# Performance work log

Hardware: AMD Instinct MI355X
Metric: run time of the kernel (lower is better)

## Reference

```python
import jax, jax.numpy as jnp
import numpy as np

N_NODES = 50000
N_EDGES = 800000
F_IN, D1, N_CLS = 128, 128, 64


def gcn_conv(x, W, b, src, dst, n):
    # x: [N, Fin] -> linear transform then normalized scatter-add aggregation
    h = x @ W  # [N, Fout]
    deg = jnp.zeros((n,), h.dtype).at[dst].add(jnp.ones((dst.shape[0],), h.dtype))
    dis = jnp.where(deg > 0, jax.lax.rsqrt(jnp.maximum(deg, 1.0)), 0.0)  # deg^-1/2, inf->0
    norm = dis[src] * dis[dst]  # [E_tot]
    msgs = norm[:, None] * h[src]  # gather source features, scale by sym norm
    out = jax.ops.segment_sum(msgs, dst, num_segments=n)  # scatter-add to targets
    return out + b


def setup_inputs() -> dict:
    key = jax.random.key(0)
    ks = jax.random.split(key, 6)
    x = jax.random.normal(ks[0], (N_NODES, F_IN), dtype=jnp.float32)
    edge_index = jax.random.randint(ks[1], (2, N_EDGES), 0, N_NODES, dtype=jnp.int64)
    W1 = jax.random.normal(ks[2], (F_IN, D1), dtype=jnp.float32) / np.sqrt(F_IN)
    b1 = jnp.zeros((D1,), dtype=jnp.float32)
    W2 = jax.random.normal(ks[3], (D1, N_CLS), dtype=jnp.float32) / np.sqrt(D1)
    b2 = jnp.zeros((N_CLS,), dtype=jnp.float32)
    return {"x": x, "edge_index": edge_index, "W1": W1, "b1": b1, "W2": W2, "b2": b2}


def reference(x, edge_index, W1, b1, W2, b2):
    n = x.shape[0]
    loops = jnp.arange(n, dtype=edge_index.dtype)
    src = jnp.concatenate([edge_index[0], loops])  # add self-loops (PyG default)
    dst = jnp.concatenate([edge_index[1], loops])
    h = gcn_conv(x, W1, b1, src, dst, n)
    h = jax.nn.relu(h)
    # F.dropout(training=self.training) is identity in eval mode
    out = gcn_conv(h, W2, b2, src, dst, n)
    return out
```

## Files before the change

### kernel.cpp

```cpp
#include <hip/hip_runtime.h>

#define NN 50000
#define NE 800000
#define CAP 64
#define NPAD 50176
#define SLICE 6250

typedef unsigned int   u32;
typedef unsigned short u16;
typedef __attribute__((ext_vector_type(8))) short short8;
typedef __attribute__((ext_vector_type(4))) float f32x4;

__device__ inline u16 f2bf(float f) {
    u32 u = __float_as_uint(f);
    return (u16)((u + 0x7FFF + ((u >> 16) & 1)) >> 16);
}
__device__ inline float bfval(u16 h) { return __uint_as_float(((u32)h) << 16); }
__device__ inline float bf_lo(u32 u) { return __uint_as_float(u << 16); }
__device__ inline float bf_hi(u32 u) { return __uint_as_float(u & 0xFFFF0000u); }


__global__ __launch_bounds__(256) void build_ell(const int* __restrict__ ei,
                                                 int* __restrict__ cnt,
                                                 u16* __restrict__ ell) {
    const int s  = blockIdx.x & 7;
    const int g  = blockIdx.x >> 3;
    const int ng = gridDim.x >> 3;
    const int lo = s * SLICE, hi = lo + SLICE;
    for (int e0 = (g * 256 + (int)threadIdx.x) * 4; e0 < NE; e0 += ng * 1024) {
        int4 d4 = *(const int4*)(ei + NE + e0);
        int dv[4] = {d4.x, d4.y, d4.z, d4.w};
#pragma unroll
        for (int k = 0; k < 4; ++k) {
            int d = dv[k];
            if (d >= lo && d < hi) {
                int src = ei[e0 + k];
                int sh = k & 1;
                int pos = atomicAdd(&cnt[sh * NPAD + d], 1);
                if (pos < 32) ell[d * CAP + sh * 32 + pos] = (u16)src;
            }
        }
    }
}


__global__ __launch_bounds__(256) void prep_w(const float* __restrict__ W1,
                                              const float* __restrict__ W2,
                                              u16* __restrict__ W1h, u16* __restrict__ W1l,
                                              u16* __restrict__ W2h, u16* __restrict__ W2l,
                                              int* __restrict__ cnt) {
    int i = blockIdx.x * 256 + threadIdx.x;
    for (int z = i; z < 2 * NPAD; z += 32768) cnt[z] = 0;
    const float* W; u16 *Dh, *Dl; int NOUT, idx;
    if (i < 16384) { W = W1; Dh = W1h; Dl = W1l; NOUT = 128; idx = i; }
    else           { idx = i - 16384; if (idx >= 8192) return;
                     W = W2; Dh = W2h; Dl = W2l; NOUT = 64; }
    int j = idx & 7, l = (idx >> 3) & 63, kc = (idx >> 9) & 3, t = idx >> 11;
    int k = kc * 32 + (l >> 4) * 8 + j;
    int n = t * 16 + (l & 15);
    float w = W[k * NOUT + n];
    u16 h = f2bf(w);
    Dh[idx] = h;
    Dl[idx] = f2bf(w - bfval(h));
}


__global__ __launch_bounds__(256) void gemm_mfma1(const float* __restrict__ A,
                                                  const u16* __restrict__ Wh,
                                                  const u16* __restrict__ Wl,
                                                  u16* __restrict__ C, int M,
                                                  const int* __restrict__ cnt,
                                                  u16* __restrict__ degT) {
    constexpr int NT = 8;
    const int tid = threadIdx.x;

    if (tid < 64) {
        int node = blockIdx.x * 64 + tid;
        if (node < NN) degT[node] = (u16)(cnt[node] + cnt[NPAD + node] + 1);
    }

    const int w = tid >> 6, l = tid & 63;
    const int m = l & 15, q = l >> 4;

    int arow = blockIdx.x * 64 + w * 16 + m;
    const float* Ar = A + (size_t)min(arow, M - 1) * 128;

    f32x4 acc[NT] = {};

#pragma unroll
    for (int kc = 0; kc < 4; ++kc) {
        float p[8];
        *(float4*)&p[0] = *(const float4*)(Ar + kc * 32 + q * 8);
        *(float4*)&p[4] = *(const float4*)(Ar + kc * 32 + q * 8 + 4);
        short8 ah, al;
#pragma unroll
        for (int j = 0; j < 8; ++j) {
            u16 h = f2bf(p[j]);
            ah[j] = (short)h;
            al[j] = (short)f2bf(p[j] - bfval(h));
        }
#pragma unroll
        for (int t = 0; t < NT; ++t) {
            size_t bo = ((size_t)(t * 4 + kc) * 64 + l) * 8;
            short8 bh = *(const short8*)(Wh + bo);
            short8 bl = *(const short8*)(Wl + bo);
            acc[t] = __builtin_amdgcn_mfma_f32_16x16x32_bf16(ah, bh, acc[t], 0, 0, 0);
            acc[t] = __builtin_amdgcn_mfma_f32_16x16x32_bf16(al, bh, acc[t], 0, 0, 0);
            acc[t] = __builtin_amdgcn_mfma_f32_16x16x32_bf16(ah, bl, acc[t], 0, 0, 0);
        }
    }

    int growbase = blockIdx.x * 64 + w * 16 + q * 4;
#pragma unroll
    for (int t = 0; t < NT; ++t)
#pragma unroll
        for (int r = 0; r < 4; ++r) {
            int grow = growbase + r;
            if (grow < M) C[(size_t)grow * 128 + t * 16 + m] = f2bf(acc[t][r]);
        }
}


__global__ __launch_bounds__(256) void gemm_mfma_bf(const u16* __restrict__ A,
                                                    const u16* __restrict__ Wh,
                                                    const u16* __restrict__ Wl,
                                                    u16* __restrict__ C, int M) {
    constexpr int NT = 4;
    const int tid = threadIdx.x;
    const int w = tid >> 6, l = tid & 63;
    const int m = l & 15, q = l >> 4;

    int arow = blockIdx.x * 64 + w * 16 + m;
    const u16* Ar = A + (size_t)min(arow, M - 1) * 128;

    f32x4 acc[NT] = {};

#pragma unroll
    for (int kc = 0; kc < 4; ++kc) {
        short8 ah = *(const short8*)(Ar + kc * 32 + q * 8);
#pragma unroll
        for (int t = 0; t < NT; ++t) {
            size_t bo = ((size_t)(t * 4 + kc) * 64 + l) * 8;
            short8 bh = *(const short8*)(Wh + bo);
            short8 bl = *(const short8*)(Wl + bo);
            acc[t] = __builtin_amdgcn_mfma_f32_16x16x32_bf16(ah, bh, acc[t], 0, 0, 0);
            acc[t] = __builtin_amdgcn_mfma_f32_16x16x32_bf16(ah, bl, acc[t], 0, 0, 0);
        }
    }

    int growbase = blockIdx.x * 64 + w * 16 + q * 4;
#pragma unroll
    for (int t = 0; t < NT; ++t)
#pragma unroll
        for (int r = 0; r < 4; ++r) {
            int grow = growbase + r;
            if (grow < M) C[(size_t)grow * 64 + t * 16 + m] = f2bf(acc[t][r]);
        }
}


template <int F, bool RELU, bool OUTBF>
__global__ __launch_bounds__(256) void aggregate_bf(const u16* __restrict__ H,
                                                    const u16* __restrict__ ell,
                                                    const int* __restrict__ cnt,
                                                    const u16* __restrict__ degT,
                                                    const float* __restrict__ bias,
                                                    void* __restrict__ outp) {
    const int tid = threadIdx.x;
    const int lane = tid & 63;
    const int wid = (int)((blockIdx.x * 256 + tid) >> 6);
    const int nw = (int)((gridDim.x * 256) >> 6);

    constexpr int L = F / 8;
    constexpr int G = 64 / L;
    const int g = lane / L;
    const int ci = lane & (L - 1);

    for (int node = wid; node < NN; node += nw) {
        const int c0r = cnt[node], c1r = cnt[NPAD + node];
        const int c0 = min(c0r, 32), c1 = min(c1r, 32);
        const int ne = min(c0 + c1, 63);
        const float di = rsqrtf((float)(c0r + c1r + 1));
        int slot = (lane < c0) ? lane : 32 + (lane - c0);
        int   s_l = (lane < ne) ? (int)ell[(size_t)node * CAP + slot] : node;
        float n_l = (lane <= ne) ? rsqrtf((float)degT[s_l]) * di : 0.0f;

        const int ng = (ne + G) / G;

        int   sC = __shfl(s_l, g);
        float nC = __shfl(n_l, g);
        uint4 vC = *(const uint4*)(H + (size_t)sC * F + ci * 8);

        float acc[8] = {0, 0, 0, 0, 0, 0, 0, 0};
        for (int gi = 0; gi < ng; ++gi) {
            int gn = min(gi + 1, ng - 1);
            int   sN = __shfl(s_l, gn * G + g);
            float nN = __shfl(n_l, gn * G + g);
            uint4 vN = *(const uint4*)(H + (size_t)sN * F + ci * 8);
            acc[0] += nC * bf_lo(vC.x); acc[1] += nC * bf_hi(vC.x);
            acc[2] += nC * bf_lo(vC.y); acc[3] += nC * bf_hi(vC.y);
            acc[4] += nC * bf_lo(vC.z); acc[5] += nC * bf_hi(vC.z);
            acc[6] += nC * bf_lo(vC.w); acc[7] += nC * bf_hi(vC.w);
            vC = vN;
            nC = (gi + 1 < ng) ? nN : 0.0f;
        }

#pragma unroll
        for (int i = 0; i < 8; ++i) {
            if (L <= 8) acc[i] += __shfl_xor(acc[i], 8);
            acc[i] += __shfl_xor(acc[i], 16);
            acc[i] += __shfl_xor(acc[i], 32);
        }

        if (lane < L) {
            float4 b0 = *(const float4*)(bias + lane * 8);
            float4 b1 = *(const float4*)(bias + lane * 8 + 4);
            float o[8] = {acc[0] + b0.x, acc[1] + b0.y, acc[2] + b0.z,
                          acc[3] + b0.w, acc[4] + b1.x, acc[5] + b1.y,
                          acc[6] + b1.z, acc[7] + b1.w};
            if (RELU)
#pragma unroll
                for (int k = 0; k < 8; ++k) o[k] = fmaxf(o[k], 0.f);
            if (OUTBF) {
                union { ushort4 s4[2]; uint4 q; } pk;
                pk.s4[0] = make_ushort4(f2bf(o[0]), f2bf(o[1]), f2bf(o[2]), f2bf(o[3]));
                pk.s4[1] = make_ushort4(f2bf(o[4]), f2bf(o[5]), f2bf(o[6]), f2bf(o[7]));
                *(uint4*)((u16*)outp + (size_t)node * F + lane * 8) = pk.q;
            } else {
                float* out = (float*)outp + (size_t)node * F + lane * 8;
                *(float4*)out = make_float4(o[0], o[1], o[2], o[3]);
                *(float4*)(out + 4) = make_float4(o[4], o[5], o[6], o[7]);
            }
        }
    }
}


extern "C" void kernel_launch(void* const* d_in, const int* in_sizes, int n_in,
                              void* d_out, int out_size, void* d_ws, size_t ws_size,
                              hipStream_t stream) {
    const float* x  = (const float*)d_in[0];
    const int*   ei = (const int*)d_in[1];
    const float* W1 = (const float*)d_in[2];
    const float* b1 = (const float*)d_in[3];
    const float* W2 = (const float*)d_in[4];
    const float* b2 = (const float*)d_in[5];
    float* out = (float*)d_out;

    char* ws = (char*)d_ws;
    size_t off = 0;
    int* cnt = (int*)ws;                     off += (size_t)2 * NPAD * 4;
    u16* ell = (u16*)(ws + off);             off += (size_t)NN * CAP * 2;
    off = (off + 255) & ~(size_t)255;
    u16* W1h = (u16*)(ws + off);             off += 16384 * 2;
    u16* W1l = (u16*)(ws + off);             off += 16384 * 2;
    u16* W2h = (u16*)(ws + off);             off += 8192 * 2;
    u16* W2l = (u16*)(ws + off);             off += 8192 * 2;
    off = (off + 255) & ~(size_t)255;
    u16* degT = (u16*)(ws + off);            off += (size_t)NPAD * 2;
    off = (off + 255) & ~(size_t)255;
    u16* Hbf = (u16*)(ws + off);             off += (size_t)NN * 128 * 2;
    u16* Abf = (u16*)(ws + off);             off += (size_t)NN * 128 * 2;
    u16* H2b = (u16*)(ws + off);             off += (size_t)NN * 64 * 2;

    prep_w<<<128, 256, 0, stream>>>(W1, W2, W1h, W1l, W2h, W2l, cnt);
    build_ell<<<1600, 256, 0, stream>>>(ei, cnt, ell);

    gemm_mfma1<<<(NN + 63) / 64, 256, 0, stream>>>(x, W1h, W1l, Hbf, NN, cnt, degT);
    aggregate_bf<128, true, true><<<2048, 256, 0, stream>>>(
        Hbf, ell, cnt, degT, b1, Abf);

    gemm_mfma_bf<<<(NN + 63) / 64, 256, 0, stream>>>(Abf, W2h, W2l, H2b, NN);
    aggregate_bf<64, false, false><<<2048, 256, 0, stream>>>(
        H2b, ell, cnt, degT, b2, out);
}
```

Measured before the change: 197.3 us.

## Compress destination indices to u16 and deepen gather prefetch in aggregation

prep_w now converts the destination row of edge_index to a 16-bit array, so the 8 slice passes in build_ell each read half as many bytes (8 dst per thread per load). The aggregation loop replaces its single-step software prefetch with a 4-deep register ring of outstanding neighbor-row loads, which should hide more gather latency. The cost is more registers per thread and an extra conversion pass inside prep_w.

```diff
diff --git a/kernel.cpp b/kernel.cpp
--- a/kernel.cpp
+++ b/kernel.cpp
@@ -21,18 +21,19 @@
 
 
 __global__ __launch_bounds__(256) void build_ell(const int* __restrict__ ei,
+                                                 const u16* __restrict__ d16,
                                                  int* __restrict__ cnt,
                                                  u16* __restrict__ ell) {
     const int s  = blockIdx.x & 7;
     const int g  = blockIdx.x >> 3;
     const int ng = gridDim.x >> 3;
     const int lo = s * SLICE, hi = lo + SLICE;
-    for (int e0 = (g * 256 + (int)threadIdx.x) * 4; e0 < NE; e0 += ng * 1024) {
-        int4 d4 = *(const int4*)(ei + NE + e0);
-        int dv[4] = {d4.x, d4.y, d4.z, d4.w};
-#pragma unroll
-        for (int k = 0; k < 4; ++k) {
-            int d = dv[k];
+    for (int e0 = (g * 256 + (int)threadIdx.x) * 8; e0 < NE; e0 += ng * 2048) {
+        union { uint4 q; u16 h[8]; } dv;
+        dv.q = *(const uint4*)(d16 + e0);
+#pragma unroll
+        for (int k = 0; k < 8; ++k) {
+            int d = dv.h[k];
             if (d >= lo && d < hi) {
                 int src = ei[e0 + k];
                 int sh = k & 1;
@@ -48,9 +49,16 @@
                                               const float* __restrict__ W2,
                                               u16* __restrict__ W1h, u16* __restrict__ W1l,
                                               u16* __restrict__ W2h, u16* __restrict__ W2l,
-                                              int* __restrict__ cnt) {
+                                              int* __restrict__ cnt,
+                                              const int* __restrict__ ei,
+                                              u16* __restrict__ d16) {
     int i = blockIdx.x * 256 + threadIdx.x;
     for (int z = i; z < 2 * NPAD; z += 32768) cnt[z] = 0;
+    for (int e = i * 4; e < NE; e += 32768 * 4) {
+        int4 d4 = *(const int4*)(ei + NE + e);
+        *(ushort4*)(d16 + e) = make_ushort4((u16)d4.x, (u16)d4.y,
+                                            (u16)d4.z, (u16)d4.w);
+    }
     const float* W; u16 *Dh, *Dl; int NOUT, idx;
     if (i < 16384) { W = W1; Dh = W1h; Dl = W1l; NOUT = 128; idx = i; }
     else           { idx = i - 16384; if (idx >= 8192) return;
@@ -173,6 +181,7 @@
 
     constexpr int L = F / 8;
     constexpr int G = 64 / L;
+    constexpr int D = 4;
     const int g = lane / L;
     const int ci = lane & (L - 1);
 
@@ -185,24 +194,37 @@
         int   s_l = (lane < ne) ? (int)ell[(size_t)node * CAP + slot] : node;
         float n_l = (lane <= ne) ? rsqrtf((float)degT[s_l]) * di : 0.0f;
 
-        const int ng = (ne + G) / G;
-
-        int   sC = __shfl(s_l, g);
-        float nC = __shfl(n_l, g);
-        uint4 vC = *(const uint4*)(H + (size_t)sC * F + ci * 8);
+        const int ngp = (ne + G) / G;
+
+        uint4 v[D]; float nn[D];
+#pragma unroll
+        for (int d = 0; d < D; ++d) {
+            int gc = min(d, ngp - 1);
+            int   sP = __shfl(s_l, gc * G + g);
+            float nP = __shfl(n_l, gc * G + g);
+            nn[d] = (d < ngp) ? nP : 0.0f;
+            v[d] = *(const uint4*)(H + (size_t)sP * F + ci * 8);
+        }
 
         float acc[8] = {0, 0, 0, 0, 0, 0, 0, 0};
-        for (int gi = 0; gi < ng; ++gi) {
-            int gn = min(gi + 1, ng - 1);
-            int   sN = __shfl(s_l, gn * G + g);
-            float nN = __shfl(n_l, gn * G + g);
-            uint4 vN = *(const uint4*)(H + (size_t)sN * F + ci * 8);
-            acc[0] += nC * bf_lo(vC.x); acc[1] += nC * bf_hi(vC.x);
-            acc[2] += nC * bf_lo(vC.y); acc[3] += nC * bf_hi(vC.y);
-            acc[4] += nC * bf_lo(vC.z); acc[5] += nC * bf_hi(vC.z);
-            acc[6] += nC * bf_lo(vC.w); acc[7] += nC * bf_hi(vC.w);
-            vC = vN;
-            nC = (gi + 1 < ng) ? nN : 0.0f;
+        const int ngR = (ngp + D - 1) & ~(D - 1);
+        for (int base = 0; base < ngR; base += D) {
+#pragma unroll
+            for (int d = 0; d < D; ++d) {
+                const float wN = nn[d];
+                const uint4 u = v[d];
+                acc[0] += wN * bf_lo(u.x); acc[1] += wN * bf_hi(u.x);
+                acc[2] += wN * bf_lo(u.y); acc[3] += wN * bf_hi(u.y);
+                acc[4] += wN * bf_lo(u.z); acc[5] += wN * bf_hi(u.z);
+                acc[6] += wN * bf_lo(u.w); acc[7] += wN * bf_hi(u.w);
+                int gn = base + D + d;
+                if (gn < ngp) {
+                    int   sN = __shfl(s_l, gn * G + g);
+                    float nN = __shfl(n_l, gn * G + g);
+                    nn[d] = nN;
+                    v[d] = *(const uint4*)(H + (size_t)sN * F + ci * 8);
+                } else nn[d] = 0.0f;
+            }
         }
 
 #pragma unroll
@@ -259,12 +281,14 @@
     off = (off + 255) & ~(size_t)255;
     u16* degT = (u16*)(ws + off);            off += (size_t)NPAD * 2;
     off = (off + 255) & ~(size_t)255;
+    u16* d16 = (u16*)(ws + off);             off += (size_t)NE * 2;
+    off = (off + 255) & ~(size_t)255;
     u16* Hbf = (u16*)(ws + off);             off += (size_t)NN * 128 * 2;
     u16* Abf = (u16*)(ws + off);             off += (size_t)NN * 128 * 2;
     u16* H2b = (u16*)(ws + off);             off += (size_t)NN * 64 * 2;
 
-    prep_w<<<128, 256, 0, stream>>>(W1, W2, W1h, W1l, W2h, W2l, cnt);
-    build_ell<<<1600, 256, 0, stream>>>(ei, cnt, ell);
+    prep_w<<<128, 256, 0, stream>>>(W1, W2, W1h, W1l, W2h, W2l, cnt, ei, d16);
+    build_ell<<<1600, 256, 0, stream>>>(ei, d16, cnt, ell);
 
     gemm_mfma1<<<(NN + 63) / 64, 256, 0, stream>>>(x, W1h, W1l, Hbf, NN, cnt, degT);
     aggregate_bf<128, true, true><<<2048, 256, 0, stream>>>(
```

Measured after the change: 213.9 us. 8.4% more time.

## Fuse ELL build with first GEMM and pack edge indices into u32

Applied to the files above, without the earlier changes.

Edge src/dst pairs are packed into a single 32-bit word in prep_w, so the ELL build reads one uint4 per four edges instead of two separate int arrays. The ELL build and the first MFMA GEMM now run as one launch with disjoint block ranges, so the atomic-heavy scatter can overlap with the dense GEMM and one launch is removed. The degT array is dropped, and aggregation recomputes degrees from cnt, which doubles the gathered loads per neighbour. The packing adds an extra pass that writes and then reads 3.2MB, and it assumes node ids fit in 16 bits.

```diff
diff --git a/kernel.cpp b/kernel.cpp
--- a/kernel.cpp
+++ b/kernel.cpp
@@ -5,6 +5,7 @@
 #define CAP 64
 #define NPAD 50176
 #define SLICE 6250
+#define NBLD 1600
 
 typedef unsigned int   u32;
 typedef unsigned short u16;
@@ -20,37 +21,25 @@
 __device__ inline float bf_hi(u32 u) { return __uint_as_float(u & 0xFFFF0000u); }
 
 
-__global__ __launch_bounds__(256) void build_ell(const int* __restrict__ ei,
-                                                 int* __restrict__ cnt,
-                                                 u16* __restrict__ ell) {
-    const int s  = blockIdx.x & 7;
-    const int g  = blockIdx.x >> 3;
-    const int ng = gridDim.x >> 3;
-    const int lo = s * SLICE, hi = lo + SLICE;
-    for (int e0 = (g * 256 + (int)threadIdx.x) * 4; e0 < NE; e0 += ng * 1024) {
-        int4 d4 = *(const int4*)(ei + NE + e0);
-        int dv[4] = {d4.x, d4.y, d4.z, d4.w};
-#pragma unroll
-        for (int k = 0; k < 4; ++k) {
-            int d = dv[k];
-            if (d >= lo && d < hi) {
-                int src = ei[e0 + k];
-                int sh = k & 1;
-                int pos = atomicAdd(&cnt[sh * NPAD + d], 1);
-                if (pos < 32) ell[d * CAP + sh * 32 + pos] = (u16)src;
-            }
-        }
-    }
-}
-
-
 __global__ __launch_bounds__(256) void prep_w(const float* __restrict__ W1,
                                               const float* __restrict__ W2,
                                               u16* __restrict__ W1h, u16* __restrict__ W1l,
                                               u16* __restrict__ W2h, u16* __restrict__ W2l,
-                                              int* __restrict__ cnt) {
+                                              int* __restrict__ cnt,
+                                              const int* __restrict__ ei,
+                                              u32* __restrict__ psd) {
     int i = blockIdx.x * 256 + threadIdx.x;
     for (int z = i; z < 2 * NPAD; z += 32768) cnt[z] = 0;
+    for (int e = i * 4; e < NE; e += 32768 * 4) {
+        int4 s4 = *(const int4*)(ei + e);
+        int4 d4 = *(const int4*)(ei + NE + e);
+        uint4 p;
+        p.x = (u32)s4.x | ((u32)d4.x << 16);
+        p.y = (u32)s4.y | ((u32)d4.y << 16);
+        p.z = (u32)s4.z | ((u32)d4.z << 16);
+        p.w = (u32)s4.w | ((u32)d4.w << 16);
+        *(uint4*)(psd + e) = p;
+    }
     const float* W; u16 *Dh, *Dl; int NOUT, idx;
     if (i < 16384) { W = W1; Dh = W1h; Dl = W1l; NOUT = 128; idx = i; }
     else           { idx = i - 16384; if (idx >= 8192) return;
@@ -65,24 +54,42 @@
 }
 
 
-__global__ __launch_bounds__(256) void gemm_mfma1(const float* __restrict__ A,
-                                                  const u16* __restrict__ Wh,
-                                                  const u16* __restrict__ Wl,
-                                                  u16* __restrict__ C, int M,
-                                                  const int* __restrict__ cnt,
-                                                  u16* __restrict__ degT) {
+__global__ __launch_bounds__(256) void fused_gb(const u32* __restrict__ psd,
+                                                int* __restrict__ cnt,
+                                                u16* __restrict__ ell,
+                                                const float* __restrict__ A,
+                                                const u16* __restrict__ Wh,
+                                                const u16* __restrict__ Wl,
+                                                u16* __restrict__ C, int M) {
+    if (blockIdx.x < NBLD) {
+        const int s  = blockIdx.x & 7;
+        const int g  = blockIdx.x >> 3;
+        const int ng = NBLD >> 3;
+        const int lo = s * SLICE, hi = lo + SLICE;
+        for (int e0 = (g * 256 + (int)threadIdx.x) * 4; e0 < NE; e0 += ng * 1024) {
+            uint4 q = *(const uint4*)(psd + e0);
+            u32 ev[4] = {q.x, q.y, q.z, q.w};
+#pragma unroll
+            for (int k = 0; k < 4; ++k) {
+                int d = (int)(ev[k] >> 16);
+                if (d >= lo && d < hi) {
+                    int src = (int)(ev[k] & 0xFFFFu);
+                    int sh = k & 1;
+                    int pos = atomicAdd(&cnt[sh * NPAD + d], 1);
+                    if (pos < 32) ell[d * CAP + sh * 32 + pos] = (u16)src;
+                }
+            }
+        }
+        return;
+    }
+
     constexpr int NT = 8;
+    const int bg = blockIdx.x - NBLD;
     const int tid = threadIdx.x;
-
-    if (tid < 64) {
-        int node = blockIdx.x * 64 + tid;
-        if (node < NN) degT[node] = (u16)(cnt[node] + cnt[NPAD + node] + 1);
-    }
-
     const int w = tid >> 6, l = tid & 63;
     const int m = l & 15, q = l >> 4;
 
-    int arow = blockIdx.x * 64 + w * 16 + m;
+    int arow = bg * 64 + w * 16 + m;
     const float* Ar = A + (size_t)min(arow, M - 1) * 128;
 
     f32x4 acc[NT] = {};
@@ -110,7 +117,7 @@
         }
     }
 
-    int growbase = blockIdx.x * 64 + w * 16 + q * 4;
+    int growbase = bg * 64 + w * 16 + q * 4;
 #pragma unroll
     for (int t = 0; t < NT; ++t)
 #pragma unroll
@@ -163,7 +170,6 @@
 __global__ __launch_bounds__(256) void aggregate_bf(const u16* __restrict__ H,
                                                     const u16* __restrict__ ell,
                                                     const int* __restrict__ cnt,
-                                                    const u16* __restrict__ degT,
                                                     const float* __restrict__ bias,
                                                     void* __restrict__ outp) {
     const int tid = threadIdx.x;
@@ -183,7 +189,9 @@
         const float di = rsqrtf((float)(c0r + c1r + 1));
         int slot = (lane < c0) ? lane : 32 + (lane - c0);
         int   s_l = (lane < ne) ? (int)ell[(size_t)node * CAP + slot] : node;
-        float n_l = (lane <= ne) ? rsqrtf((float)degT[s_l]) * di : 0.0f;
+        float n_l = (lane <= ne)
+                        ? rsqrtf((float)(cnt[s_l] + cnt[NPAD + s_l] + 1)) * di
+                        : 0.0f;
 
         const int ng = (ne + G) / G;
 
@@ -257,20 +265,20 @@
     u16* W2h = (u16*)(ws + off);             off += 8192 * 2;
     u16* W2l = (u16*)(ws + off);             off += 8192 * 2;
     off = (off + 255) & ~(size_t)255;
-    u16* degT = (u16*)(ws + off);            off += (size_t)NPAD * 2;
+    u32* psd = (u32*)(ws + off);             off += (size_t)NE * 4;
     off = (off + 255) & ~(size_t)255;
     u16* Hbf = (u16*)(ws + off);             off += (size_t)NN * 128 * 2;
     u16* Abf = (u16*)(ws + off);             off += (size_t)NN * 128 * 2;
     u16* H2b = (u16*)(ws + off);             off += (size_t)NN * 64 * 2;
 
-    prep_w<<<128, 256, 0, stream>>>(W1, W2, W1h, W1l, W2h, W2l, cnt);
-    build_ell<<<1600, 256, 0, stream>>>(ei, cnt, ell);
-
-    gemm_mfma1<<<(NN + 63) / 64, 256, 0, stream>>>(x, W1h, W1l, Hbf, NN, cnt, degT);
-    aggregate_bf<128, true, true><<<2048, 256, 0, stream>>>(
-        Hbf, ell, cnt, degT, b1, Abf);
-
-    gemm_mfma_bf<<<(NN + 63) / 64, 256, 0, stream>>>(Abf, W2h, W2l, H2b, NN);
-    aggregate_bf<64, false, false><<<2048, 256, 0, stream>>>(
-        H2b, ell, cnt, degT, b2, out);
-}
+    const int NBG = (NN + 63) / 64;
+
+    prep_w<<<128, 256, 0, stream>>>(W1, W2, W1h, W1l, W2h, W2l, cnt, ei, psd);
+
+    fused_gb<<<NBLD + NBG, 256, 0, stream>>>(psd, cnt, ell, x, W1h, W1l, Hbf, NN);
+
+    aggregate_bf<128, true, true><<<2048, 256, 0, stream>>>(Hbf, ell, cnt, b1, Abf);
+
+    gemm_mfma_bf<<<NBG, 256, 0, stream>>>(Abf, W2h, W2l, H2b, NN);
+    aggregate_bf<64, false, false><<<2048, 256, 0, stream>>>(H2b, ell, cnt, b2, out);
+}
```

New measurement: 193.8 us. About the same (-1.8%).
